# Performance work log

Measured on AMD Instinct MI355X. Metric: run time of the kernel, lower is better.

Reference implementation:

```python
import jax, jax.numpy as jnp
import numpy as np
from jax import lax

B, TIN, N, TOUT, C = 8, 168, 1500, 24, 16
EMB, ALPHA, BETA, TOPK, DEPTH = 16, 1.5, 0.2, 12, 2
KERNELS = (2, 3, 6, 7)


def setup_inputs() -> dict:
    key = jax.random.key(0)
    ks = jax.random.split(key, 32)
    def rn(k, shape, scale=0.1):
        return jax.random.normal(k, shape, jnp.float32) * scale
    inp = {"x": jax.random.normal(ks[0], (B, TIN, N, 1), jnp.float32)}
    inp["pw"], inp["pb"] = rn(ks[1], (C, 1)), rn(ks[2], (C,))
    branch = C // len(KERNELS)
    for i, k in enumerate(KERNELS):
        inp[f"tw{k}"] = rn(ks[3 + 2 * i], (branch, C, 1, k))
        inp[f"tb{k}"] = rn(ks[4 + 2 * i], (branch,))
    inp["e1"], inp["e2"] = rn(ks[11], (N, EMB), 1.0), rn(ks[12], (N, EMB), 1.0)
    inp["gw1"], inp["gb1"] = rn(ks[13], (EMB, EMB)), rn(ks[14], (EMB,))
    inp["gw2"], inp["gb2"] = rn(ks[15], (EMB, EMB)), rn(ks[16], (EMB,))
    inp["mw"], inp["mb"] = rn(ks[17], (C, (DEPTH + 1) * C)), rn(ks[18], (C,))
    inp["rw1"], inp["rb1"] = rn(ks[19], (C, C)), rn(ks[20], (C,))
    inp["rw2"], inp["rb2"] = rn(ks[21], (TOUT, C)), rn(ks[22], (TOUT,))
    return inp


def _conv1x1(h, w, b):
    # h: [B, Cin, N, T], w: [Cout, Cin], b: [Cout]
    return jnp.einsum('bint,oi->bont', h, w) + b[None, :, None, None]


def _forward(x, pw, pb, tw2, tb2, tw3, tb3, tw6, tb6, tw7, tb7,
             e1, e2, gw1, gb1, gw2, gb2, mw, mb, rw1, rb1, rw2, rb2):
    h = jnp.transpose(x, (0, 3, 2, 1))                      # [B,1,N,TIN]
    h = _conv1x1(h, pw, pb)                                 # [B,C,N,TIN]
    # dilated inception: branches with kernels (2,3,6,7), truncate to shortest
    tlen = TIN - max(KERNELS) + 1
    outs = []
    for w, b in ((tw2, tb2), (tw3, tb3), (tw6, tb6), (tw7, tb7)):
        o = lax.conv_general_dilated(h, w, (1, 1), 'VALID',
                                     dimension_numbers=('NCHW', 'OIHW', 'NCHW'))
        outs.append(o[..., -tlen:] + b[None, :, None, None])
    h = jax.nn.relu(jnp.concatenate(outs, axis=1))          # [B,C,N,tlen]
    # adaptive top-k graph learning
    m1 = jnp.tanh(ALPHA * (e1 @ gw1 + gb1))
    m2 = jnp.tanh(ALPHA * (e2 @ gw2 + gb2))
    a = jax.nn.relu(jnp.tanh(ALPHA * (m1 @ m2.T - m2 @ m1.T)))  # [N,N]
    _, idx = lax.top_k(a, TOPK)
    mask = jnp.zeros((N, N), jnp.float32).at[jnp.arange(N)[:, None], idx].set(1.0)
    adj = a * mask
    # mix-hop graph convolution with row-normalized (A + I)
    adj = adj + jnp.eye(N, dtype=jnp.float32)
    adj = adj / jnp.sum(adj, axis=1, keepdims=True)
    hin = h
    hops = [h]
    for _ in range(DEPTH):
        h = BETA * hin + (1.0 - BETA) * jnp.einsum('bcwt,vw->bcvt', h, adj)
        hops.append(h)
    ho = jnp.concatenate(hops, axis=1)                      # [B,(D+1)C,N,tlen]
    h = jax.nn.relu(_conv1x1(ho, mw, mb))                   # [B,C,N,tlen]
    # dropout -> identity at inference
    r = jax.nn.relu(_conv1x1(h, rw1, rb1))
    y = _conv1x1(r, rw2, rb2)                               # [B,TOUT,N,tlen]
    return jnp.mean(y, axis=-1)                             # [B,TOUT,N]


def reference(x, pw, pb, tw2, tb2, tw3, tb3, tw6, tb6, tw7, tb7,
              e1, e2, gw1, gb1, gw2, gb2, mw, mb, rw1, rb1, rw2, rb2):
    return _forward(x, pw, pb, tw2, tb2, tw3, tb3, tw6, tb6, tw7, tb7,
                    e1, e2, gw1, gb1, gw2, gb2, mw, mb, rw1, rb1, rw2, rb2)
```

## Files before the change

kernel.cpp:

```cpp
#include <hip/hip_runtime.h>

#define BB 8
#define TIN 168
#define NN 1500
#define TOUTC 24
#define TLEN 162
#define NG 32
#define NTH 1024
#define SN 2
#define TOPKK 12
#define NTILE 94
#define NPAD 1504

#define OFF_M1   0
#define OFF_M2   24000
#define OFF_M1T  48000
#define OFF_M2T  72000
#define OFF_EW   96000
#define OFF_EB   96112
#define OFF_ADJ  96128
#define OFF_FR   135128
#define OFF_PART 328664

typedef __attribute__((ext_vector_type(8))) _Float16 half8;
typedef __attribute__((ext_vector_type(4))) _Float16 half4v;
typedef __attribute__((ext_vector_type(2))) _Float16 half2v;
typedef __attribute__((ext_vector_type(4))) float v4f;

__device__ __forceinline__ unsigned int pk2(float lo, float hi) {
    return __builtin_bit_cast(unsigned int, __builtin_amdgcn_cvt_pkrtz(lo, hi));
}
__device__ __forceinline__ float h2lo(unsigned int u) {
    return (float)__builtin_bit_cast(half2v, u).x;
}
__device__ __forceinline__ float h2hi(unsigned int u) {
    return (float)__builtin_bit_cast(half2v, u).y;
}
__device__ __forceinline__ half2v as_h2(unsigned int u) { return __builtin_bit_cast(half2v, u); }
__device__ __forceinline__ unsigned int as_u(half2v h) { return __builtin_bit_cast(unsigned int, h); }
__device__ __forceinline__ half8 as_h8(uint4 u) { return __builtin_bit_cast(half8, u); }

__global__ __launch_bounds__(256) void prep_kernel(
    const float* __restrict__ e1, const float* __restrict__ e2,
    const float* __restrict__ gw1, const float* __restrict__ gb1,
    const float* __restrict__ gw2, const float* __restrict__ gb2,
    const float* __restrict__ pw, const float* __restrict__ pb,
    const float* __restrict__ tw2, const float* __restrict__ tb2,
    const float* __restrict__ tw3, const float* __restrict__ tb3,
    const float* __restrict__ tw6, const float* __restrict__ tb6,
    const float* __restrict__ tw7, const float* __restrict__ tb7,
    const float* __restrict__ mw, const float* __restrict__ rw1,
    float* __restrict__ ws)
{
    int n = blockIdx.x * blockDim.x + threadIdx.x;
    if (n < NN) {
        float a1[16], a2[16];
        #pragma unroll
        for (int o = 0; o < 16; ++o) { a1[o] = gb1[o]; a2[o] = gb2[o]; }
        #pragma unroll
        for (int i = 0; i < 16; ++i) {
            float u = e1[n*16+i], v = e2[n*16+i];
            #pragma unroll
            for (int o = 0; o < 16; ++o) {
                a1[o] += u * gw1[i*16+o];
                a2[o] += v * gw2[i*16+o];
            }
        }
        #pragma unroll
        for (int o = 0; o < 16; ++o) {
            float t1v = tanhf(1.5f*a1[o]);
            float t2v = tanhf(1.5f*a2[o]);
            ws[OFF_M1 + n*16+o] = t1v;
            ws[OFF_M2 + n*16+o] = t2v;
            ws[OFF_M1T + o*NN + n] = t1v;
            ws[OFF_M2T + o*NN + n] = t2v;
        }
    }
    if (blockIdx.x == 0 && threadIdx.x < 16) {
        int c = threadIdx.x;
        int br = c >> 2, oc = c & 3;
        const float* tw; const float* tb; int k;
        if (br == 0)      { tw = tw2; tb = tb2; k = 2; }
        else if (br == 1) { tw = tw3; tb = tb3; k = 3; }
        else if (br == 2) { tw = tw6; tb = tb6; k = 6; }
        else              { tw = tw7; tb = tb7; k = 7; }
        for (int d = 0; d < 7; ++d) ws[OFF_EW + c*7 + d] = 0.f;
        float ebv = tb[oc];
        for (int j = 0; j < k; ++j) {
            float s = 0.f, sb = 0.f;
            for (int ic = 0; ic < 16; ++ic) {
                float w = tw[(oc*16+ic)*k + j];
                s  += w * pw[ic];
                sb += w * pb[ic];
            }
            ws[OFF_EW + c*7 + (7-k+j)] = s;
            ebv += sb;
        }
        ws[OFF_EB + c] = ebv;
    }
    if (blockIdx.x == 1 && threadIdx.x < 64) {
        int lane = threadIdx.x;
        int m = lane & 15, qq = lane >> 4;
        unsigned short* frw = (unsigned short*)(ws + OFF_FR);
        for (int j = 0; j < 8; ++j) {
            int k = qq*8 + j;
            float s = (k < 16) ? mw[m*48+k] + 0.2f*(mw[m*48+16+k] + mw[m*48+32+k])
                               : 0.8f*mw[m*48+16+(k-16)] + 0.16f*mw[m*48+32+(k-16)];
            _Float16 hi = (_Float16)s;
            _Float16 lo = (_Float16)(s - (float)hi);
            frw[0*512 + lane*8 + j] = __builtin_bit_cast(unsigned short, hi);
            frw[1*512 + lane*8 + j] = __builtin_bit_cast(unsigned short, lo);
        }
        for (int j = 0; j < 4; ++j) {
            int k = qq*4 + j;
            float sv = 0.64f*mw[m*48+32+k];
            float sr = rw1[m*16+k];
            _Float16 vhi = (_Float16)sv;
            _Float16 vlo = (_Float16)(sv - (float)vhi);
            _Float16 rhi = (_Float16)sr;
            _Float16 rlo = (_Float16)(sr - (float)rhi);
            frw[2*512 + lane*4 + j] = __builtin_bit_cast(unsigned short, vhi);
            frw[3*512 + lane*4 + j] = __builtin_bit_cast(unsigned short, vlo);
            frw[4*512 + lane*4 + j] = __builtin_bit_cast(unsigned short, rhi);
            frw[5*512 + lane*4 + j] = __builtin_bit_cast(unsigned short, rlo);
        }
    }
}

__global__ __launch_bounds__(256) void graph_kernel(
    const float* __restrict__ m1, const float* __restrict__ m2,
    const float* __restrict__ m1T, const float* __restrict__ m2T,
    int2* __restrict__ adj)
{
    int v = blockIdx.x;
    int tid = threadIdx.x;
    __shared__ float wv4[4];
    __shared__ int   wi4[4];
    __shared__ int   bcast_i;
    __shared__ float m1v[16], m2v[16];
    if (tid < 16) { m1v[tid] = m1[v*16+tid]; m2v[tid] = m2[v*16+tid]; }
    __syncthreads();
    float sreg[6];
    #pragma unroll
    for (int u = 0; u < 6; ++u) {
        int j = tid + 256*u;
        float a = -1.f;
        if (j < NN) {
            float d = 0.f;
            #pragma unroll
            for (int i = 0; i < 16; ++i)
                d += m1v[i]*m2T[i*NN+j] - m2v[i]*m1T[i*NN+j];
            float t = tanhf(1.5f*d);
            a = t > 0.f ? t : 0.f;
        }
        sreg[u] = a;
    }
    float lb = -1.f; int li = NN;
    #pragma unroll
    for (int u = 0; u < 6; ++u) {
        int j = tid + 256*u;
        if (j < NN && sreg[u] > lb) { lb = sreg[u]; li = j; }
    }
    const int wid = tid >> 6;
    float kw[TOPKK]; int ki[TOPKK];
    #pragma unroll
    for (int it = 0; it < TOPKK; ++it) {
        float bv = lb; int bi = li;
        #pragma unroll
        for (int off = 32; off > 0; off >>= 1) {
            float ov = __shfl_down(bv, off);
            int   oi = __shfl_down(bi, off);
            if (ov > bv || (ov == bv && oi < bi)) { bv = ov; bi = oi; }
        }
        if ((tid & 63) == 0) { wv4[wid] = bv; wi4[wid] = bi; }
        __syncthreads();
        if (tid == 0) {
            #pragma unroll
            for (int w = 1; w < 4; ++w) {
                float ov = wv4[w]; int oi = wi4[w];
                if (ov > bv || (ov == bv && oi < bi)) { bv = ov; bi = oi; }
            }
            kw[it] = bv; ki[it] = bi;
            bcast_i = bi;
        }
        __syncthreads();
        int win = bcast_i;
        if (li == win) {
            #pragma unroll
            for (int u = 0; u < 6; ++u)
                if (tid + 256*u == win) sreg[u] = -1.f;
            lb = -1.f; li = NN;
            #pragma unroll
            for (int u = 0; u < 6; ++u) {
                int j = tid + 256*u;
                if (j < NN && sreg[u] > lb) { lb = sreg[u]; li = j; }
            }
        }
    }
    if (tid == 0) {
        float s = 1.f;
        #pragma unroll
        for (int it = 0; it < TOPKK; ++it) s += kw[it];
        float inv = 1.f/s;
        #pragma unroll
        for (int it = 0; it < TOPKK; ++it) {
            float w = kw[it]*inv;
            adj[it*NN + v] = make_int2((int)pk2(w, w), ki[it]);
        }
        adj[TOPKK*NN + v] = make_int2((int)pk2(inv, inv), v);
    }
}

__device__ __forceinline__ half8 ldfrag(const unsigned short* fr, int plane, int lane) {
    const uint4* p = (const uint4*)(fr + plane*512);
    return as_h8(p[lane]);
}
__device__ __forceinline__ half4v ldfrag4(const unsigned short* fr, int plane, int lane) {
    const uint2* p = (const uint2*)(fr + plane*512);
    return __builtin_bit_cast(half4v, p[lane]);
}

__global__ __launch_bounds__(NTH, 4) void main_kernel(
    const float* __restrict__ x,
    const float* __restrict__ ew, const float* __restrict__ eb,
    const int2* __restrict__ adj,
    const unsigned short* __restrict__ fr,
    unsigned int* __restrict__ part,
    const float* __restrict__ mb, const float* __restrict__ rb1)
{
    __shared__ uint4 feat[6][NPAD];

    const int tid = threadIdx.x;
    const int lane = tid & 63;
    const int wid = tid >> 6;
    const int b = blockIdx.x >> 5;
    const int g = blockIdx.x & 31;
    const int t0 = (g*TLEN) >> 5;
    const int t1 = ((g+1)*TLEN) >> 5;
    const int n0 = lane & 15, q = lane >> 4;
    unsigned int* partBG = part + (size_t)(b*NG + g)*NN*8;

    #pragma unroll 1
    for (int s = 0; s < SN; ++s) {
        int v = tid + NTH*s;
        if (v < NN) {
            float xv[7];
            #pragma unroll
            for (int d = 0; d < 7; ++d) xv[d] = x[(b*TIN + t0 + d)*NN + v];
            float h[16];
            #pragma unroll
            for (int c = 0; c < 16; ++c) {
                float a = eb[c];
                #pragma unroll
                for (int d = 0; d < 7; ++d) a += ew[c*7+d]*xv[d];
                h[c] = a > 0.f ? a : 0.f;
            }
            feat[0][v] = make_uint4(pk2(h[0],h[1]), pk2(h[2],h[3]), pk2(h[4],h[5]), pk2(h[6],h[7]));
            feat[1][v] = make_uint4(pk2(h[8],h[9]), pk2(h[10],h[11]), pk2(h[12],h[13]), pk2(h[14],h[15]));
        }
    }
    __syncthreads();

    for (int t = t0; t < t1; ++t) {
        const int par = (t - t0) & 1;
        const int hc = par ? 4 : 0;
        const int hn = par ? 0 : 4;

        #pragma unroll 1
        for (int s = 0; s < SN; ++s) {
            int v = tid + NTH*s;
            if (v < NN) {
                const half2v zero = {(_Float16)0.f, (_Float16)0.f};
                half2v acc[8];
                #pragma unroll
                for (int i = 0; i < 8; ++i) acc[i] = zero;
                #pragma unroll
                for (int j = 0; j < 13; ++j) {
                    int2 aw = adj[j*NN + v];
                    half2v w2 = as_h2((unsigned int)aw.x);
                    int nb = aw.y;
                    uint4 b0 = feat[hc][nb], b1 = feat[hc+1][nb];
                    acc[0] = as_h2(b0.x) * w2 + acc[0];
                    acc[1] = as_h2(b0.y) * w2 + acc[1];
                    acc[2] = as_h2(b0.z) * w2 + acc[2];
                    acc[3] = as_h2(b0.w) * w2 + acc[3];
                    acc[4] = as_h2(b1.x) * w2 + acc[4];
                    acc[5] = as_h2(b1.y) * w2 + acc[5];
                    acc[6] = as_h2(b1.z) * w2 + acc[6];
                    acc[7] = as_h2(b1.w) * w2 + acc[7];
                }
                feat[2][v] = make_uint4(as_u(acc[0]), as_u(acc[1]), as_u(acc[2]), as_u(acc[3]));
                feat[3][v] = make_uint4(as_u(acc[4]), as_u(acc[5]), as_u(acc[6]), as_u(acc[7]));
            }
        }
        __syncthreads();

        if (t + 1 < t1) {
            #pragma unroll 1
            for (int s = 0; s < SN; ++s) {
                int v = tid + NTH*s;
                if (v < NN) {
                    float xv[7];
                    #pragma unroll
                    for (int d = 0; d < 7; ++d) xv[d] = x[(b*TIN + (t+1) + d)*NN + v];
                    float h[16];
                    #pragma unroll
                    for (int c = 0; c < 16; ++c) {
                        float a = eb[c];
                        #pragma unroll
                        for (int d = 0; d < 7; ++d) a += ew[c*7+d]*xv[d];
                        h[c] = a > 0.f ? a : 0.f;
                    }
                    feat[hn][v]   = make_uint4(pk2(h[0],h[1]), pk2(h[2],h[3]), pk2(h[4],h[5]), pk2(h[6],h[7]));
                    feat[hn+1][v] = make_uint4(pk2(h[8],h[9]), pk2(h[10],h[11]), pk2(h[12],h[13]), pk2(h[14],h[15]));
                }
            }
        }
        {
            half8  a1h = ldfrag(fr, 0, lane),  a1l = ldfrag(fr, 1, lane);
            half4v v2h = ldfrag4(fr, 2, lane), v2l = ldfrag4(fr, 3, lane);
            half4v r1h = ldfrag4(fr, 4, lane), r1l = ldfrag4(fr, 5, lane);
            float mbq[4], rbq[4];
            #pragma unroll
            for (int r = 0; r < 4; ++r) { mbq[r] = mb[q*4+r]; rbq[r] = rb1[q*4+r]; }
            const uint2* uH = (const uint2*)feat[2 + (q >> 1)];
            #pragma unroll 1
            for (int T = wid; T < NTILE; T += 16) {
                int n = T*16 + n0;
                half8 bf = as_h8(feat[(q < 2) ? (hc + q) : q][n]);
                v4f z = {0.f,0.f,0.f,0.f};
                z = __builtin_amdgcn_mfma_f32_16x16x32_f16(a1h, bf, z, 0, 0, 0);
                z = __builtin_amdgcn_mfma_f32_16x16x32_f16(a1l, bf, z, 0, 0, 0);
                int vc = n < NN ? n : NN-1;
                const half2v zero = {(_Float16)0.f, (_Float16)0.f};
                half2v ga = zero, gb = zero;
                #pragma unroll
                for (int j = 0; j < 13; ++j) {
                    int2 aw = adj[j*NN + vc];
                    half2v w2 = as_h2((unsigned int)aw.x);
                    int nb = aw.y;
                    uint2 ps = uH[nb*2 + (q & 1)];
                    ga = as_h2(ps.x) * w2 + ga;
                    gb = as_h2(ps.y) * w2 + gb;
                }
                half4v w4 = {ga.x, ga.y, gb.x, gb.y};
                v4f sv = {0.f,0.f,0.f,0.f};
                sv = __builtin_amdgcn_mfma_f32_16x16x16f16(v2h, w4, sv, 0, 0, 0);
                sv = __builtin_amdgcn_mfma_f32_16x16x16f16(v2l, w4, sv, 0, 0, 0);
                float y0 = mbq[0] + z[0] + sv[0];
                float y1 = mbq[1] + z[1] + sv[1];
                float y2 = mbq[2] + z[2] + sv[2];
                float y3 = mbq[3] + z[3] + sv[3];
                y0 = y0 > 0.f ? y0 : 0.f;  y1 = y1 > 0.f ? y1 : 0.f;
                y2 = y2 > 0.f ? y2 : 0.f;  y3 = y3 > 0.f ? y3 : 0.f;
                uint2 yk; yk.x = pk2(y0, y1); yk.y = pk2(y2, y3);
                half4v y4 = __builtin_bit_cast(half4v, yk);
                v4f acc = {0.f,0.f,0.f,0.f};
                acc = __builtin_amdgcn_mfma_f32_16x16x16f16(r1h, y4, acc, 0, 0, 0);
                acc = __builtin_amdgcn_mfma_f32_16x16x16f16(r1l, y4, acc, 0, 0, 0);
                if (n < NN) {
                    float r0 = acc[0]+rbq[0], r1 = acc[1]+rbq[1], r2 = acc[2]+rbq[2], r3 = acc[3]+rbq[3];
                    r0 = r0 > 0.f ? r0 : 0.f;  r1 = r1 > 0.f ? r1 : 0.f;
                    r2 = r2 > 0.f ? r2 : 0.f;  r3 = r3 > 0.f ? r3 : 0.f;
                    uint2 nv; nv.x = pk2(r0, r1); nv.y = pk2(r2, r3);
                    uint2* pp = (uint2*)(partBG + (size_t)n*8 + q*2);
                    if (t == t0) {
                        *pp = nv;
                    } else {
                        uint2 o = *pp;
                        uint2 m;
                        m.x = as_u(as_h2(o.x) + as_h2(nv.x));
                        m.y = as_u(as_h2(o.y) + as_h2(nv.y));
                        *pp = m;
                    }
                }
            }
        }
        __syncthreads();
    }
}

__global__ __launch_bounds__(256) void reduce_kernel(const unsigned int* __restrict__ part,
                                                     const float* __restrict__ rw2,
                                                     const float* __restrict__ rb2,
                                                     float* __restrict__ out)
{
    int idx = blockIdx.x*256 + threadIdx.x;
    if (idx >= BB*NN) return;
    int v = idx % NN;
    int b = idx / NN;
    float s[16];
    #pragma unroll
    for (int c = 0; c < 16; ++c) s[c] = 0.f;
    #pragma unroll 4
    for (int g = 0; g < NG; ++g) {
        const uint4* p4 = (const uint4*)(part + ((size_t)(b*NG + g)*NN + v)*8);
        uint4 u0 = p4[0], u1 = p4[1];
        s[0] += h2lo(u0.x); s[1] += h2hi(u0.x); s[2]  += h2lo(u0.y); s[3]  += h2hi(u0.y);
        s[4] += h2lo(u0.z); s[5] += h2hi(u0.z); s[6]  += h2lo(u0.w); s[7]  += h2hi(u0.w);
        s[8] += h2lo(u1.x); s[9] += h2hi(u1.x); s[10] += h2lo(u1.y); s[11] += h2hi(u1.y);
        s[12]+= h2lo(u1.z); s[13]+= h2hi(u1.z); s[14] += h2lo(u1.w); s[15] += h2hi(u1.w);
    }
    #pragma unroll
    for (int c = 0; c < 16; ++c) s[c] *= (1.0f/TLEN);
    #pragma unroll
    for (int o = 0; o < TOUTC; ++o) {
        float a = rb2[o];
        #pragma unroll
        for (int c = 0; c < 16; ++c) a += rw2[o*16+c]*s[c];
        out[(b*TOUTC + o)*NN + v] = a;
    }
}

extern "C" void kernel_launch(void* const* d_in, const int* in_sizes, int n_in,
                              void* d_out, int out_size, void* d_ws, size_t ws_size,
                              hipStream_t stream)
{
    const float* x   = (const float*)d_in[0];
    const float* pw  = (const float*)d_in[1];
    const float* pb  = (const float*)d_in[2];
    const float* tw2 = (const float*)d_in[3];
    const float* tb2 = (const float*)d_in[4];
    const float* tw3 = (const float*)d_in[5];
    const float* tb3 = (const float*)d_in[6];
    const float* tw6 = (const float*)d_in[7];
    const float* tb6 = (const float*)d_in[8];
    const float* tw7 = (const float*)d_in[9];
    const float* tb7 = (const float*)d_in[10];
    const float* e1  = (const float*)d_in[11];
    const float* e2  = (const float*)d_in[12];
    const float* gw1 = (const float*)d_in[13];
    const float* gb1 = (const float*)d_in[14];
    const float* gw2 = (const float*)d_in[15];
    const float* gb2 = (const float*)d_in[16];
    const float* mw  = (const float*)d_in[17];
    const float* mb  = (const float*)d_in[18];
    const float* rw1 = (const float*)d_in[19];
    const float* rb1 = (const float*)d_in[20];
    const float* rw2 = (const float*)d_in[21];
    const float* rb2 = (const float*)d_in[22];
    float* ws  = (float*)d_ws;
    float* out = (float*)d_out;

    prep_kernel<<<(NN + 255)/256, 256, 0, stream>>>(e1,e2,gw1,gb1,gw2,gb2,pw,pb,
                                                    tw2,tb2,tw3,tb3,tw6,tb6,tw7,tb7,
                                                    mw, rw1, ws);
    graph_kernel<<<NN, 256, 0, stream>>>(ws + OFF_M1, ws + OFF_M2,
                                         ws + OFF_M1T, ws + OFF_M2T,
                                         (int2*)(ws + OFF_ADJ));
    main_kernel<<<BB*NG, NTH, 0, stream>>>(x, ws + OFF_EW, ws + OFF_EB,
                                           (const int2*)(ws + OFF_ADJ),
                                           (const unsigned short*)(ws + OFF_FR),
                                           (unsigned int*)(ws + OFF_PART), mb, rb1);
    reduce_kernel<<<(BB*NN + 255)/256, 256, 0, stream>>>((const unsigned int*)(ws + OFF_PART),
                                                         rw2, rb2, out);
}
```

Before: 281.4 us.

## Accumulate per-timestep partial outputs in registers and write once per block

Each wave now owns a fixed contiguous chunk of 94 nodes (6 tiles) across all timesteps instead of a strided assignment. Per-timestep results are summed in fp32 registers rather than read-modify-written to global memory every timestep, with a single store at the end. This removes repeated global loads and stores and also changes the accumulation from fp16 to fp32. In exchange it adds register pressure under launch bounds of 1024 threads. Waves with out-of-range tiles also compute redundant clamped tiles.

```diff
diff --git a/kernel.cpp b/kernel.cpp
--- a/kernel.cpp
+++ b/kernel.cpp
@@ -7,10 +7,10 @@
 #define TLEN 162
 #define NG 32
 #define NTH 1024
-#define SN 2
 #define TOPKK 12
 #define NTILE 94
 #define NPAD 1504
+#define WCHUNK 94
 
 #define OFF_M1   0
 #define OFF_M2   24000
@@ -238,12 +238,14 @@
     const int t0 = (g*TLEN) >> 5;
     const int t1 = ((g+1)*TLEN) >> 5;
     const int n0 = lane & 15, q = lane >> 4;
+    const int wbase = wid * WCHUNK;
     unsigned int* partBG = part + (size_t)(b*NG + g)*NN*8;
 
     #pragma unroll 1
-    for (int s = 0; s < SN; ++s) {
-        int v = tid + NTH*s;
-        if (v < NN) {
+    for (int s = 0; s < 2; ++s) {
+        int l2 = 64*s + lane;
+        int v = wbase + l2;
+        if (l2 < WCHUNK && v < NN) {
             float xv[7];
             #pragma unroll
             for (int d = 0; d < 7; ++d) xv[d] = x[(b*TIN + t0 + d)*NN + v];
@@ -261,15 +263,22 @@
     }
     __syncthreads();
 
+    float rp[6][4];
+    #pragma unroll
+    for (int it = 0; it < 6; ++it)
+        #pragma unroll
+        for (int r = 0; r < 4; ++r) rp[it][r] = 0.f;
+
     for (int t = t0; t < t1; ++t) {
         const int par = (t - t0) & 1;
         const int hc = par ? 4 : 0;
         const int hn = par ? 0 : 4;
 
         #pragma unroll 1
-        for (int s = 0; s < SN; ++s) {
-            int v = tid + NTH*s;
-            if (v < NN) {
+        for (int s = 0; s < 2; ++s) {
+            int l2 = 64*s + lane;
+            int v = wbase + l2;
+            if (l2 < WCHUNK && v < NN) {
                 const half2v zero = {(_Float16)0.f, (_Float16)0.f};
                 half2v acc[8];
                 #pragma unroll
@@ -297,9 +306,10 @@
 
         if (t + 1 < t1) {
             #pragma unroll 1
-            for (int s = 0; s < SN; ++s) {
-                int v = tid + NTH*s;
-                if (v < NN) {
+            for (int s = 0; s < 2; ++s) {
+                int l2 = 64*s + lane;
+                int v = wbase + l2;
+                if (l2 < WCHUNK && v < NN) {
                     float xv[7];
                     #pragma unroll
                     for (int d = 0; d < 7; ++d) xv[d] = x[(b*TIN + (t+1) + d)*NN + v];
@@ -324,9 +334,11 @@
             #pragma unroll
             for (int r = 0; r < 4; ++r) { mbq[r] = mb[q*4+r]; rbq[r] = rb1[q*4+r]; }
             const uint2* uH = (const uint2*)feat[2 + (q >> 1)];
-            #pragma unroll 1
-            for (int T = wid; T < NTILE; T += 16) {
-                int n = T*16 + n0;
+            #pragma unroll
+            for (int it = 0; it < 6; ++it) {
+                int T = wid*6 + it;
+                int Tc = T < NTILE ? T : NTILE-1;
+                int n = Tc*16 + n0;
                 half8 bf = as_h8(feat[(q < 2) ? (hc + q) : q][n]);
                 v4f z = {0.f,0.f,0.f,0.f};
                 z = __builtin_amdgcn_mfma_f32_16x16x32_f16(a1h, bf, z, 0, 0, 0);
@@ -358,25 +370,24 @@
                 v4f acc = {0.f,0.f,0.f,0.f};
                 acc = __builtin_amdgcn_mfma_f32_16x16x16f16(r1h, y4, acc, 0, 0, 0);
                 acc = __builtin_amdgcn_mfma_f32_16x16x16f16(r1l, y4, acc, 0, 0, 0);
-                if (n < NN) {
-                    float r0 = acc[0]+rbq[0], r1 = acc[1]+rbq[1], r2 = acc[2]+rbq[2], r3 = acc[3]+rbq[3];
-                    r0 = r0 > 0.f ? r0 : 0.f;  r1 = r1 > 0.f ? r1 : 0.f;
-                    r2 = r2 > 0.f ? r2 : 0.f;  r3 = r3 > 0.f ? r3 : 0.f;
-                    uint2 nv; nv.x = pk2(r0, r1); nv.y = pk2(r2, r3);
-                    uint2* pp = (uint2*)(partBG + (size_t)n*8 + q*2);
-                    if (t == t0) {
-                        *pp = nv;
-                    } else {
-                        uint2 o = *pp;
-                        uint2 m;
-                        m.x = as_u(as_h2(o.x) + as_h2(nv.x));
-                        m.y = as_u(as_h2(o.y) + as_h2(nv.y));
-                        *pp = m;
-                    }
-                }
+                float r0 = acc[0]+rbq[0], r1 = acc[1]+rbq[1], r2 = acc[2]+rbq[2], r3 = acc[3]+rbq[3];
+                rp[it][0] += r0 > 0.f ? r0 : 0.f;
+                rp[it][1] += r1 > 0.f ? r1 : 0.f;
+                rp[it][2] += r2 > 0.f ? r2 : 0.f;
+                rp[it][3] += r3 > 0.f ? r3 : 0.f;
             }
         }
         __syncthreads();
+    }
+
+    #pragma unroll
+    for (int it = 0; it < 6; ++it) {
+        int T = wid*6 + it;
+        int n = T*16 + n0;
+        if (T < NTILE && n < NN) {
+            uint2 nv; nv.x = pk2(rp[it][0], rp[it][1]); nv.y = pk2(rp[it][2], rp[it][3]);
+            *(uint2*)(partBG + (size_t)n*8 + q*2) = nv;
+        }
     }
 }
 
```

New measurement: 464.9 us. 65.2% more time.

## Process four graph rows per block in graph kernel, sharing column loads

Applied to the files above, without the earlier changes.

The graph kernel now handles four adjacency rows per block, so each load of m1T/m2T columns feeds four dot products. Scores go to shared memory, and the top-k selection rescans them every round for all four rows, replacing the earlier register-resident incremental approach. This cuts global traffic and the block count, but each top-k round now rescans shared memory, and there are four times fewer blocks.

```diff
diff --git a/kernel.cpp b/kernel.cpp
--- a/kernel.cpp
+++ b/kernel.cpp
@@ -11,6 +11,7 @@
 #define TOPKK 12
 #define NTILE 94
 #define NPAD 1504
+#define GNPB 4
 
 #define OFF_M1   0
 #define OFF_M2   24000
@@ -132,80 +133,95 @@
     const float* __restrict__ m1T, const float* __restrict__ m2T,
     int2* __restrict__ adj)
 {
-    int v = blockIdx.x;
-    int tid = threadIdx.x;
-    __shared__ float wv4[4];
-    __shared__ int   wi4[4];
-    __shared__ int   bcast_i;
-    __shared__ float m1v[16], m2v[16];
-    if (tid < 16) { m1v[tid] = m1[v*16+tid]; m2v[tid] = m2[v*16+tid]; }
+    __shared__ float s_lds[GNPB][1536];
+    __shared__ float m1v4[GNPB][16], m2v4[GNPB][16];
+    __shared__ float wred_v[GNPB][4];
+    __shared__ int   wred_i[GNPB][4];
+    __shared__ float winw[GNPB][TOPKK];
+    __shared__ int   wini[GNPB][TOPKK];
+
+    const int v0 = blockIdx.x * GNPB;
+    const int tid = threadIdx.x;
+    const int lane = tid & 63;
+    const int wv = tid >> 6;
+
+    if (tid < GNPB*16) {
+        int k = tid >> 4, i = tid & 15;
+        m1v4[k][i] = m1[(v0+k)*16 + i];
+        m2v4[k][i] = m2[(v0+k)*16 + i];
+    }
     __syncthreads();
-    float sreg[6];
+
     #pragma unroll
     for (int u = 0; u < 6; ++u) {
         int j = tid + 256*u;
-        float a = -1.f;
+        float d0 = 0.f, d1 = 0.f, d2 = 0.f, d3 = 0.f;
         if (j < NN) {
-            float d = 0.f;
-            #pragma unroll
-            for (int i = 0; i < 16; ++i)
-                d += m1v[i]*m2T[i*NN+j] - m2v[i]*m1T[i*NN+j];
-            float t = tanhf(1.5f*d);
-            a = t > 0.f ? t : 0.f;
-        }
-        sreg[u] = a;
-    }
-    float lb = -1.f; int li = NN;
-    #pragma unroll
-    for (int u = 0; u < 6; ++u) {
-        int j = tid + 256*u;
-        if (j < NN && sreg[u] > lb) { lb = sreg[u]; li = j; }
-    }
-    const int wid = tid >> 6;
-    float kw[TOPKK]; int ki[TOPKK];
-    #pragma unroll
+            #pragma unroll
+            for (int i = 0; i < 16; ++i) {
+                float a2t = m2T[i*NN+j];
+                float a1t = m1T[i*NN+j];
+                d0 += m1v4[0][i]*a2t - m2v4[0][i]*a1t;
+                d1 += m1v4[1][i]*a2t - m2v4[1][i]*a1t;
+                d2 += m1v4[2][i]*a2t - m2v4[2][i]*a1t;
+                d3 += m1v4[3][i]*a2t - m2v4[3][i]*a1t;
+            }
+            float t0 = tanhf(1.5f*d0), t1 = tanhf(1.5f*d1);
+            float t2 = tanhf(1.5f*d2), t3 = tanhf(1.5f*d3);
+            s_lds[0][j] = t0 > 0.f ? t0 : 0.f;
+            s_lds[1][j] = t1 > 0.f ? t1 : 0.f;
+            s_lds[2][j] = t2 > 0.f ? t2 : 0.f;
+            s_lds[3][j] = t3 > 0.f ? t3 : 0.f;
+        } else {
+            s_lds[0][j] = -1.f; s_lds[1][j] = -1.f;
+            s_lds[2][j] = -1.f; s_lds[3][j] = -1.f;
+        }
+    }
+    __syncthreads();
+
     for (int it = 0; it < TOPKK; ++it) {
-        float bv = lb; int bi = li;
-        #pragma unroll
-        for (int off = 32; off > 0; off >>= 1) {
-            float ov = __shfl_down(bv, off);
-            int   oi = __shfl_down(bi, off);
-            if (ov > bv || (ov == bv && oi < bi)) { bv = ov; bi = oi; }
-        }
-        if ((tid & 63) == 0) { wv4[wid] = bv; wi4[wid] = bi; }
-        __syncthreads();
-        if (tid == 0) {
-            #pragma unroll
-            for (int w = 1; w < 4; ++w) {
-                float ov = wv4[w]; int oi = wi4[w];
-                if (ov > bv || (ov == bv && oi < bi)) { bv = ov; bi = oi; }
-            }
-            kw[it] = bv; ki[it] = bi;
-            bcast_i = bi;
-        }
-        __syncthreads();
-        int win = bcast_i;
-        if (li == win) {
-            #pragma unroll
-            for (int u = 0; u < 6; ++u)
-                if (tid + 256*u == win) sreg[u] = -1.f;
-            lb = -1.f; li = NN;
+        #pragma unroll
+        for (int k = 0; k < GNPB; ++k) {
+            float lb = -2.f; int li = 0;
             #pragma unroll
             for (int u = 0; u < 6; ++u) {
                 int j = tid + 256*u;
-                if (j < NN && sreg[u] > lb) { lb = sreg[u]; li = j; }
-            }
-        }
-    }
-    if (tid == 0) {
+                float val = s_lds[k][j];
+                if (val > lb) { lb = val; li = j; }
+            }
+            #pragma unroll
+            for (int off = 32; off > 0; off >>= 1) {
+                float ov = __shfl_down(lb, off);
+                int   oi = __shfl_down(li, off);
+                if (ov > lb || (ov == lb && oi < li)) { lb = ov; li = oi; }
+            }
+            if (lane == 0) { wred_v[k][wv] = lb; wred_i[k][wv] = li; }
+        }
+        __syncthreads();
+        if (tid < GNPB) {
+            int k = tid;
+            float bv = wred_v[k][0]; int bi = wred_i[k][0];
+            #pragma unroll
+            for (int w = 1; w < 4; ++w) {
+                float ov = wred_v[k][w]; int oi = wred_i[k][w];
+                if (ov > bv || (ov == bv && oi < bi)) { bv = ov; bi = oi; }
+            }
+            winw[k][it] = bv; wini[k][it] = bi;
+            s_lds[k][bi] = -1.f;
+        }
+        __syncthreads();
+    }
+
+    if (tid < GNPB) {
+        int k = tid; int v = v0 + k;
         float s = 1.f;
         #pragma unroll
-        for (int it = 0; it < TOPKK; ++it) s += kw[it];
+        for (int it = 0; it < TOPKK; ++it) s += winw[k][it];
         float inv = 1.f/s;
         #pragma unroll
         for (int it = 0; it < TOPKK; ++it) {
-            float w = kw[it]*inv;
-            adj[it*NN + v] = make_int2((int)pk2(w, w), ki[it]);
+            float w = winw[k][it]*inv;
+            adj[it*NN + v] = make_int2((int)pk2(w, w), wini[k][it]);
         }
         adj[TOPKK*NN + v] = make_int2((int)pk2(inv, inv), v);
     }
@@ -445,9 +461,9 @@
     prep_kernel<<<(NN + 255)/256, 256, 0, stream>>>(e1,e2,gw1,gb1,gw2,gb2,pw,pb,
                                                     tw2,tb2,tw3,tb3,tw6,tb6,tw7,tb7,
                                                     mw, rw1, ws);
-    graph_kernel<<<NN, 256, 0, stream>>>(ws + OFF_M1, ws + OFF_M2,
-                                         ws + OFF_M1T, ws + OFF_M2T,
-                                         (int2*)(ws + OFF_ADJ));
+    graph_kernel<<<(NN + GNPB - 1)/GNPB, 256, 0, stream>>>(ws + OFF_M1, ws + OFF_M2,
+                                                           ws + OFF_M1T, ws + OFF_M2T,
+                                                           (int2*)(ws + OFF_ADJ));
     main_kernel<<<BB*NG, NTH, 0, stream>>>(x, ws + OFF_EW, ws + OFF_EB,
                                            (const int2*)(ws + OFF_ADJ),
                                            (const unsigned short*)(ws + OFF_FR),
```

Result: slower. 431.7 us (+53.4%).
